# Kernel tuning notes

Measured on AMD Instinct MI355X. Metric: run time of the kernel, lower is better.

The kernel has to match this reference:

```python
import jax, jax.numpy as jnp
import numpy as np


def _linear(x, w, b=None):
    # torch nn.Linear: y = x @ W^T + b, W has shape [out, in]
    y = jnp.einsum('...i,oi->...o', x, w)
    return y if b is None else y + b


def setup_inputs() -> dict:
    key = jax.random.key(0)
    ks = jax.random.split(key, 20)
    B, S = 2048, 128

    def w(k, out_d, in_d):
        bound = 1.0 / np.sqrt(in_d)
        return jax.random.uniform(k, (out_d, in_d), jnp.float32, -bound, bound)

    def bias(k, out_d, in_d):
        bound = 1.0 / np.sqrt(in_d)
        return jax.random.uniform(k, (out_d,), jnp.float32, -bound, bound)

    return {
        'x': jax.random.normal(ks[0], (B, S, 8), jnp.float32),
        'w_fm': w(ks[1], 16, 8),  'b_fm': bias(ks[2], 16, 8),
        'w_c1': w(ks[3], 16, 16), 'b_c1': bias(ks[4], 16, 16),
        'w_p1': w(ks[5], 12, 16), 'b_p1': bias(ks[6], 12, 16),
        'w_c2': w(ks[7], 8, 12),  'b_c2': bias(ks[8], 8, 12),
        'w_p2': w(ks[9], 4, 8),   'b_p2': bias(ks[10], 4, 8),
        'w_c3': w(ks[11], 4, 4),  'b_c3': bias(ks[12], 4, 4),
        'w_q': w(ks[13], 4, 4),
        'w_k': w(ks[14], 4, 4),
        'w_v': w(ks[15], 4, 4),
        'w_fc': w(ks[16], 1, 4),  'b_fc': bias(ks[17], 1, 4),
    }


def reference(x, w_fm, b_fm, w_c1, b_c1, w_p1, b_p1, w_c2, b_c2,
              w_p2, b_p2, w_c3, b_c3, w_q, w_k, w_v, w_fc, b_fc):
    EMBED_DIM = 4
    h = jnp.tanh(_linear(x, w_fm, b_fm))   # [B,S,16]
    h = jnp.tanh(_linear(h, w_c1, b_c1))   # [B,S,16]
    h = jnp.tanh(_linear(h, w_p1, b_p1))   # [B,S,12]
    h = jnp.tanh(_linear(h, w_c2, b_c2))   # [B,S,8]
    h = jnp.tanh(_linear(h, w_p2, b_p2))   # [B,S,4]
    h = jnp.tanh(_linear(h, w_c3, b_c3))   # [B,S,4]
    # self-attention over sequence axis
    q = _linear(h, w_q)                     # [B,S,4]
    k = _linear(h, w_k)
    v = _linear(h, w_v)
    scores = jnp.einsum('bqd,bkd->bqk', q, k) / np.sqrt(EMBED_DIM)
    attn = jax.nn.softmax(scores, axis=-1)  # [B,S,S]
    h = jnp.einsum('bqk,bkd->bqd', attn, v) # [B,S,4]
    out = _linear(h, w_fc, b_fc)            # [B,S,1]
    return jax.nn.sigmoid(out)
```

## Files before the change

### kernel.cpp

```cpp
#include <hip/hip_runtime.h>

#define DEV __device__ __forceinline__

typedef _Float16 h2 __attribute__((ext_vector_type(2)));

DEV float fast_rcp(float x) { return __builtin_amdgcn_rcpf(x); }

DEV float fexp2(float x) {
#if __has_builtin(__builtin_amdgcn_exp2f)
    return __builtin_amdgcn_exp2f(x);
#else
    float r; asm("v_exp_f32 %0, %1" : "=v"(r) : "v"(x)); return r;
#endif
}

DEV float dot2acc(h2 a, h2 b, float c) {
#if __has_builtin(__builtin_amdgcn_fdot2)
    return __builtin_amdgcn_fdot2(a, b, c, false);
#else
    return c + (float)a.x * (float)b.x + (float)a.y * (float)b.y;
#endif
}

DEV float fast_tanh(float x) {
    float e = fexp2(x * 2.885390082f);
    return 1.0f - 2.0f * fast_rcp(e + 1.0f);
}
DEV float fast_sigmoid(float x) {
    return fast_rcp(1.0f + fexp2(x * -1.442695041f));
}

template <int IN, int OUT, bool HAS_BIAS, bool TANH>
DEV void layer(const float* __restrict__ w, const float* __restrict__ b,
               const float (&in)[IN], float (&out)[OUT]) {
    #pragma unroll
    for (int o = 0; o < OUT; ++o) {
        float acc = HAS_BIAS ? b[o] : 0.0f;
        #pragma unroll
        for (int i = 0; i < IN; ++i) acc = fmaf(in[i], w[o * IN + i], acc);
        out[o] = TANH ? fast_tanh(acc) : acc;
    }
}

__global__ __launch_bounds__(256)
void qcnn_fused_kernel(const float* __restrict__ x,
                       const float* __restrict__ w_fm, const float* __restrict__ b_fm,
                       const float* __restrict__ w_c1, const float* __restrict__ b_c1,
                       const float* __restrict__ w_p1, const float* __restrict__ b_p1,
                       const float* __restrict__ w_c2, const float* __restrict__ b_c2,
                       const float* __restrict__ w_p2, const float* __restrict__ b_p2,
                       const float* __restrict__ w_c3, const float* __restrict__ b_c3,
                       const float* __restrict__ w_q,  const float* __restrict__ w_k,
                       const float* __restrict__ w_v,
                       const float* __restrict__ w_fc, const float* __restrict__ b_fc,
                       float* __restrict__ out) {
    const int t     = threadIdx.x;
    const int bb    = t >> 7;
    const int tok   = t & 127;
    const int batch = blockIdx.x * 2 + bb;

    __shared__ uint4 kvbuf[2][128];

    const float* xp = x + ((size_t)batch * 128 + tok) * 8;
    float4 x0 = *reinterpret_cast<const float4*>(xp);
    float4 x1 = *reinterpret_cast<const float4*>(xp + 4);
    float xin[8] = {x0.x, x0.y, x0.z, x0.w, x1.x, x1.y, x1.z, x1.w};

    float h1[16], h2a[16], h3[12], h4[8], h5[4], h6[4];
    layer<8, 16, true, true>(w_fm, b_fm, xin, h1);
    layer<16, 16, true, true>(w_c1, b_c1, h1, h2a);
    layer<16, 12, true, true>(w_p1, b_p1, h2a, h3);
    layer<12, 8, true, true>(w_c2, b_c2, h3, h4);
    layer<8, 4, true, true>(w_p2, b_p2, h4, h5);
    layer<4, 4, true, true>(w_c3, b_c3, h5, h6);

    float qv[4], kk[4];
    layer<4, 4, false, false>(w_q, nullptr, h6, qv);
    layer<4, 4, false, false>(w_k, nullptr, h6, kk);

    float wf[4];
    #pragma unroll
    for (int i = 0; i < 4; ++i)
        wf[i] = fmaf(w_fc[0], w_v[0 * 4 + i],
                fmaf(w_fc[1], w_v[1 * 4 + i],
                fmaf(w_fc[2], w_v[2 * 4 + i], w_fc[3] * w_v[3 * 4 + i])));
    float u = fmaf(wf[0], h6[0], fmaf(wf[1], h6[1], fmaf(wf[2], h6[2], wf[3] * h6[3])));

    h2 pk01 = {(_Float16)kk[0], (_Float16)kk[1]};
    h2 pk23 = {(_Float16)kk[2], (_Float16)kk[3]};
    uint4 ent;
    ent.x = __builtin_bit_cast(unsigned, pk01);
    ent.y = __builtin_bit_cast(unsigned, pk23);
    ent.z = __builtin_bit_cast(unsigned, u);
    ent.w = 0;
    kvbuf[bb][tok] = ent;

    const float QS = 0.7213475204f;
    h2 q01 = {(_Float16)(qv[0] * QS), (_Float16)(qv[1] * QS)};
    h2 q23 = {(_Float16)(qv[2] * QS), (_Float16)(qv[3] * QS)};

    __syncthreads();

    unsigned q01u = __builtin_bit_cast(unsigned, q01);
    unsigned q23u = __builtin_bit_cast(unsigned, q23);
    unsigned q01o = __shfl_xor(q01u, 1);
    unsigned q23o = __shfl_xor(q23u, 1);
    const bool odd = (t & 1);
    h2 q01_r0 = __builtin_bit_cast(h2, odd ? q01o : q01u);
    h2 q23_r0 = __builtin_bit_cast(h2, odd ? q23o : q23u);
    h2 q01_r1 = __builtin_bit_cast(h2, odd ? q01u : q01o);
    h2 q23_r1 = __builtin_bit_cast(h2, odd ? q23u : q23o);

    const uint4* __restrict__ base = kvbuf[bb] + (odd ? 64 : 0);
    float d0 = 0.f, d1 = 0.f, s0acc = 0.f, s1acc = 0.f;
    #pragma unroll 8
    for (int j = 0; j < 64; ++j) {
        uint4 c = base[j];
        h2 k01 = __builtin_bit_cast(h2, c.x);
        h2 k23 = __builtin_bit_cast(h2, c.y);
        float uj = __builtin_bit_cast(float, c.z);
        float s0 = dot2acc(q01_r0, k01, dot2acc(q23_r0, k23, 0.f));
        float s1 = dot2acc(q01_r1, k01, dot2acc(q23_r1, k23, 0.f));
        float e0 = fexp2(s0);
        float e1 = fexp2(s1);
        d0 += e0;                 d1 += e1;
        s0acc = fmaf(e0, uj, s0acc);
        s1acc = fmaf(e1, uj, s1acc);
    }
    d0    += __shfl_xor(d0, 1);    d1    += __shfl_xor(d1, 1);
    s0acc += __shfl_xor(s0acc, 1); s1acc += __shfl_xor(s1acc, 1);

    float dd = odd ? d1 : d0;
    float uu = odd ? s1acc : s0acc;
    float z = uu * fast_rcp(dd) + b_fc[0];
    out[(size_t)batch * 128 + tok] = fast_sigmoid(z);
}

extern "C" void kernel_launch(void* const* d_in, const int* in_sizes, int n_in,
                              void* d_out, int out_size, void* d_ws, size_t ws_size,
                              hipStream_t stream) {
    const float* x    = (const float*)d_in[0];
    const float* w_fm = (const float*)d_in[1];
    const float* b_fm = (const float*)d_in[2];
    const float* w_c1 = (const float*)d_in[3];
    const float* b_c1 = (const float*)d_in[4];
    const float* w_p1 = (const float*)d_in[5];
    const float* b_p1 = (const float*)d_in[6];
    const float* w_c2 = (const float*)d_in[7];
    const float* b_c2 = (const float*)d_in[8];
    const float* w_p2 = (const float*)d_in[9];
    const float* b_p2 = (const float*)d_in[10];
    const float* w_c3 = (const float*)d_in[11];
    const float* b_c3 = (const float*)d_in[12];
    const float* w_q  = (const float*)d_in[13];
    const float* w_k  = (const float*)d_in[14];
    const float* w_v  = (const float*)d_in[15];
    const float* w_fc = (const float*)d_in[16];
    const float* b_fc = (const float*)d_in[17];
    float* out = (float*)d_out;

    dim3 grid(1024);
    dim3 block(256);
    qcnn_fused_kernel<<<grid, block, 0, stream>>>(
        x, w_fm, b_fm, w_c1, b_c1, w_p1, b_p1, w_c2, b_c2,
        w_p2, b_p2, w_c3, b_c3, w_q, w_k, w_v, w_fc, b_fc, out);
}
```

Measured before the change: 21.36 us.

## Assign two tokens per thread with one batch per wavefront

Each thread now runs the MLP head for two tokens and computes full 128-key attention for both queries. This replaces the earlier scheme where thread pairs split the key range and combined results with lane shuffles. Blocks hold four batches and the grid is halved. This removes the shuffles and selects and amortizes weight reads, but halves the thread count and lengthens each thread's serial work, which reduces latency hiding.

```diff
diff --git a/kernel.cpp b/kernel.cpp
--- a/kernel.cpp
+++ b/kernel.cpp
@@ -42,6 +42,41 @@
     }
 }
 
+DEV void token_head(const float (&xin)[8],
+                    const float* __restrict__ w_fm, const float* __restrict__ b_fm,
+                    const float* __restrict__ w_c1, const float* __restrict__ b_c1,
+                    const float* __restrict__ w_p1, const float* __restrict__ b_p1,
+                    const float* __restrict__ w_c2, const float* __restrict__ b_c2,
+                    const float* __restrict__ w_p2, const float* __restrict__ b_p2,
+                    const float* __restrict__ w_c3, const float* __restrict__ b_c3,
+                    const float* __restrict__ w_q,  const float* __restrict__ w_k,
+                    const float (&wf)[4],
+                    h2& q01, h2& q23, uint4& ent) {
+    float h1[16], h2a[16], h3[12], h4[8], h5[4], h6[4];
+    layer<8, 16, true, true>(w_fm, b_fm, xin, h1);
+    layer<16, 16, true, true>(w_c1, b_c1, h1, h2a);
+    layer<16, 12, true, true>(w_p1, b_p1, h2a, h3);
+    layer<12, 8, true, true>(w_c2, b_c2, h3, h4);
+    layer<8, 4, true, true>(w_p2, b_p2, h4, h5);
+    layer<4, 4, true, true>(w_c3, b_c3, h5, h6);
+
+    float qv[4], kk[4];
+    layer<4, 4, false, false>(w_q, nullptr, h6, qv);
+    layer<4, 4, false, false>(w_k, nullptr, h6, kk);
+    float u = fmaf(wf[0], h6[0], fmaf(wf[1], h6[1], fmaf(wf[2], h6[2], wf[3] * h6[3])));
+
+    h2 pk01 = {(_Float16)kk[0], (_Float16)kk[1]};
+    h2 pk23 = {(_Float16)kk[2], (_Float16)kk[3]};
+    ent.x = __builtin_bit_cast(unsigned, pk01);
+    ent.y = __builtin_bit_cast(unsigned, pk23);
+    ent.z = __builtin_bit_cast(unsigned, u);
+    ent.w = 0;
+
+    const float QS = 0.7213475204f;
+    q01 = h2{(_Float16)(qv[0] * QS), (_Float16)(qv[1] * QS)};
+    q23 = h2{(_Float16)(qv[2] * QS), (_Float16)(qv[3] * QS)};
+}
+
 __global__ __launch_bounds__(256)
 void qcnn_fused_kernel(const float* __restrict__ x,
                        const float* __restrict__ w_fm, const float* __restrict__ b_fm,
@@ -55,28 +90,11 @@
                        const float* __restrict__ w_fc, const float* __restrict__ b_fc,
                        float* __restrict__ out) {
     const int t     = threadIdx.x;
-    const int bb    = t >> 7;
-    const int tok   = t & 127;
-    const int batch = blockIdx.x * 2 + bb;
+    const int bb    = t >> 6;
+    const int lane  = t & 63;
+    const int batch = blockIdx.x * 4 + bb;
 
-    __shared__ uint4 kvbuf[2][128];
-
-    const float* xp = x + ((size_t)batch * 128 + tok) * 8;
-    float4 x0 = *reinterpret_cast<const float4*>(xp);
-    float4 x1 = *reinterpret_cast<const float4*>(xp + 4);
-    float xin[8] = {x0.x, x0.y, x0.z, x0.w, x1.x, x1.y, x1.z, x1.w};
-
-    float h1[16], h2a[16], h3[12], h4[8], h5[4], h6[4];
-    layer<8, 16, true, true>(w_fm, b_fm, xin, h1);
-    layer<16, 16, true, true>(w_c1, b_c1, h1, h2a);
-    layer<16, 12, true, true>(w_p1, b_p1, h2a, h3);
-    layer<12, 8, true, true>(w_c2, b_c2, h3, h4);
-    layer<8, 4, true, true>(w_p2, b_p2, h4, h5);
-    layer<4, 4, true, true>(w_c3, b_c3, h5, h6);
-
-    float qv[4], kk[4];
-    layer<4, 4, false, false>(w_q, nullptr, h6, qv);
-    layer<4, 4, false, false>(w_k, nullptr, h6, kk);
+    __shared__ uint4 kvbuf[4][128];
 
     float wf[4];
     #pragma unroll
@@ -84,56 +102,48 @@
         wf[i] = fmaf(w_fc[0], w_v[0 * 4 + i],
                 fmaf(w_fc[1], w_v[1 * 4 + i],
                 fmaf(w_fc[2], w_v[2 * 4 + i], w_fc[3] * w_v[3 * 4 + i])));
-    float u = fmaf(wf[0], h6[0], fmaf(wf[1], h6[1], fmaf(wf[2], h6[2], wf[3] * h6[3])));
 
-    h2 pk01 = {(_Float16)kk[0], (_Float16)kk[1]};
-    h2 pk23 = {(_Float16)kk[2], (_Float16)kk[3]};
-    uint4 ent;
-    ent.x = __builtin_bit_cast(unsigned, pk01);
-    ent.y = __builtin_bit_cast(unsigned, pk23);
-    ent.z = __builtin_bit_cast(unsigned, u);
-    ent.w = 0;
-    kvbuf[bb][tok] = ent;
+    const float* xpA = x + ((size_t)batch * 128 + lane) * 8;
+    const float* xpB = xpA + 64 * 8;
+    float4 a0 = *reinterpret_cast<const float4*>(xpA);
+    float4 a1 = *reinterpret_cast<const float4*>(xpA + 4);
+    float4 b0 = *reinterpret_cast<const float4*>(xpB);
+    float4 b1 = *reinterpret_cast<const float4*>(xpB + 4);
+    float xA[8] = {a0.x, a0.y, a0.z, a0.w, a1.x, a1.y, a1.z, a1.w};
+    float xB[8] = {b0.x, b0.y, b0.z, b0.w, b1.x, b1.y, b1.z, b1.w};
 
-    const float QS = 0.7213475204f;
-    h2 q01 = {(_Float16)(qv[0] * QS), (_Float16)(qv[1] * QS)};
-    h2 q23 = {(_Float16)(qv[2] * QS), (_Float16)(qv[3] * QS)};
+    h2 qA01, qA23, qB01, qB23;
+    uint4 entA, entB;
+    token_head(xA, w_fm, b_fm, w_c1, b_c1, w_p1, b_p1, w_c2, b_c2,
+               w_p2, b_p2, w_c3, b_c3, w_q, w_k, wf, qA01, qA23, entA);
+    token_head(xB, w_fm, b_fm, w_c1, b_c1, w_p1, b_p1, w_c2, b_c2,
+               w_p2, b_p2, w_c3, b_c3, w_q, w_k, wf, qB01, qB23, entB);
 
+    kvbuf[bb][lane]      = entA;
+    kvbuf[bb][lane + 64] = entB;
     __syncthreads();
 
-    unsigned q01u = __builtin_bit_cast(unsigned, q01);
-    unsigned q23u = __builtin_bit_cast(unsigned, q23);
-    unsigned q01o = __shfl_xor(q01u, 1);
-    unsigned q23o = __shfl_xor(q23u, 1);
-    const bool odd = (t & 1);
-    h2 q01_r0 = __builtin_bit_cast(h2, odd ? q01o : q01u);
-    h2 q23_r0 = __builtin_bit_cast(h2, odd ? q23o : q23u);
-    h2 q01_r1 = __builtin_bit_cast(h2, odd ? q01u : q01o);
-    h2 q23_r1 = __builtin_bit_cast(h2, odd ? q23u : q23o);
-
-    const uint4* __restrict__ base = kvbuf[bb] + (odd ? 64 : 0);
-    float d0 = 0.f, d1 = 0.f, s0acc = 0.f, s1acc = 0.f;
+    float dA = 0.f, dB = 0.f, uA = 0.f, uB = 0.f;
     #pragma unroll 8
-    for (int j = 0; j < 64; ++j) {
-        uint4 c = base[j];
+    for (int j = 0; j < 128; ++j) {
+        uint4 c = kvbuf[bb][j];
         h2 k01 = __builtin_bit_cast(h2, c.x);
         h2 k23 = __builtin_bit_cast(h2, c.y);
         float uj = __builtin_bit_cast(float, c.z);
-        float s0 = dot2acc(q01_r0, k01, dot2acc(q23_r0, k23, 0.f));
-        float s1 = dot2acc(q01_r1, k01, dot2acc(q23_r1, k23, 0.f));
-        float e0 = fexp2(s0);
-        float e1 = fexp2(s1);
-        d0 += e0;                 d1 += e1;
-        s0acc = fmaf(e0, uj, s0acc);
-        s1acc = fmaf(e1, uj, s1acc);
+        float sA = dot2acc(qA01, k01, dot2acc(qA23, k23, 0.f));
+        float sB = dot2acc(qB01, k01, dot2acc(qB23, k23, 0.f));
+        float eA = fexp2(sA);
+        float eB = fexp2(sB);
+        dA += eA;  dB += eB;
+        uA = fmaf(eA, uj, uA);
+        uB = fmaf(eB, uj, uB);
     }
-    d0    += __shfl_xor(d0, 1);    d1    += __shfl_xor(d1, 1);
-    s0acc += __shfl_xor(s0acc, 1); s1acc += __shfl_xor(s1acc, 1);
 
-    float dd = odd ? d1 : d0;
-    float uu = odd ? s1acc : s0acc;
-    float z = uu * fast_rcp(dd) + b_fc[0];
-    out[(size_t)batch * 128 + tok] = fast_sigmoid(z);
+    float zA = uA * fast_rcp(dA) + b_fc[0];
+    float zB = uB * fast_rcp(dB) + b_fc[0];
+    float* op = out + (size_t)batch * 128 + lane;
+    op[0]  = fast_sigmoid(zA);
+    op[64] = fast_sigmoid(zB);
 }
 
 extern "C" void kernel_launch(void* const* d_in, const int* in_sizes, int n_in,
@@ -159,7 +169,7 @@
     const float* b_fc = (const float*)d_in[17];
     float* out = (float*)d_out;
 
-    dim3 grid(1024);
+    dim3 grid(512);
     dim3 block(256);
     qcnn_fused_kernel<<<grid, block, 0, stream>>>(
         x, w_fm, b_fm, w_c1, b_c1, w_p1, b_p1, w_c2, b_c2,
```

Result: slower. 22.20 us (+4.0%).
